# Kernel optimization log

Hardware: AMD Instinct MI355X
Metric: run time of the kernel (lower is better)

## Reference

```python
import jax, jax.numpy as jnp
import numpy as np

EPS = 1e-5
N_NODES = 50000


def sage_conv(x, src, dst, Wl, Wr, b):
    # mean-aggregate source features at destination nodes, then two linears
    msgs = x[src]  # [E, F] irregular gather
    agg = jax.ops.segment_sum(msgs, dst, num_segments=N_NODES)
    cnt = jax.ops.segment_sum(jnp.ones((src.shape[0], 1), x.dtype), dst,
                              num_segments=N_NODES)
    agg = agg / jnp.maximum(cnt, 1.0)
    return agg @ Wl + x @ Wr + b


def batch_norm(h, gamma, beta):
    mu = jnp.mean(h, axis=0)
    var = jnp.mean((h - mu) ** 2, axis=0)  # biased var, as torch BN training
    return (h - mu) * jax.lax.rsqrt(var + EPS) * gamma + beta


def setup_inputs() -> dict:
    key = jax.random.key(0)
    ks = jax.random.split(key, 16)
    d_in, d_h, n_cls, n_edges = 128, 128, 2, 600000
    s = lambda fan: 1.0 / np.sqrt(fan)
    inp = {
        "x": jax.random.normal(ks[0], (N_NODES, d_in), jnp.float32),
        "edge_index": jax.random.randint(ks[1], (2, n_edges), 0, N_NODES, jnp.int64),
        "W_l0": jax.random.uniform(ks[2], (d_in, d_h), jnp.float32, -s(d_in), s(d_in)),
        "W_r0": jax.random.uniform(ks[3], (d_in, d_h), jnp.float32, -s(d_in), s(d_in)),
        "b0": jnp.zeros((d_h,), jnp.float32),
        "g0": jnp.ones((d_h,), jnp.float32),
        "be0": jnp.zeros((d_h,), jnp.float32),
        "W_l1": jax.random.uniform(ks[4], (d_h, d_h), jnp.float32, -s(d_h), s(d_h)),
        "W_r1": jax.random.uniform(ks[5], (d_h, d_h), jnp.float32, -s(d_h), s(d_h)),
        "b1": jnp.zeros((d_h,), jnp.float32),
        "g1": jnp.ones((d_h,), jnp.float32),
        "be1": jnp.zeros((d_h,), jnp.float32),
        "W_out": jax.random.uniform(ks[6], (d_h, n_cls), jnp.float32, -s(d_h), s(d_h)),
        "b_out": jnp.zeros((n_cls,), jnp.float32),
    }
    return inp


def reference(x, edge_index, W_l0, W_r0, b0, g0, be0,
              W_l1, W_r1, b1, g1, be1, W_out, b_out):
    src, dst = edge_index[0], edge_index[1]
    # layer 0: SAGEConv -> BN -> ReLU (dropout = identity in eval/reference)
    h = sage_conv(x, src, dst, W_l0, W_r0, b0)
    h = jax.nn.relu(batch_norm(h, g0, be0))
    # layer 1
    h = sage_conv(h, src, dst, W_l1, W_r1, b1)
    h = jax.nn.relu(batch_norm(h, g1, be1))
    return h @ W_out + b_out
```

## Files before the change

### kernel.cpp

```cpp
#include <hip/hip_runtime.h>
#include <hip/hip_bf16.h>

#define F 128

typedef __attribute__((ext_vector_type(8))) short short8;
typedef __attribute__((ext_vector_type(4))) float floatx4;

__device__ __forceinline__ float bf_lo(unsigned u) { return __uint_as_float(u << 16); }
__device__ __forceinline__ float bf_hi(unsigned u) { return __uint_as_float(u & 0xffff0000u); }

__device__ __forceinline__ unsigned short f2bf(float x) {
  unsigned u = __float_as_uint(x);
  u += 0x7fffu + ((u >> 16) & 1u);
  return (unsigned short)(u >> 16);
}
__device__ __forceinline__ unsigned pack2(float a, float b) {
  return (unsigned)f2bf(a) | ((unsigned)f2bf(b) << 16);
}
__device__ __forceinline__ void add8(float* a, uint4 u) {
  a[0] += bf_lo(u.x); a[1] += bf_hi(u.x);
  a[2] += bf_lo(u.y); a[3] += bf_hi(u.y);
  a[4] += bf_lo(u.z); a[5] += bf_hi(u.z);
  a[6] += bf_lo(u.w); a[7] += bf_hi(u.w);
}

__global__ __launch_bounds__(256) void k_pre(const int* __restrict__ dst, int* __restrict__ A,
                                             int E, int cb,
                                             const float* __restrict__ x,
                                             const float* __restrict__ Wl0,
                                             const float* __restrict__ Wr0,
                                             const float* __restrict__ Wl1,
                                             const float* __restrict__ Wr1,
                                             unsigned short* __restrict__ xb,
                                             unsigned short* __restrict__ WcatT0,
                                             unsigned short* __restrict__ WcatT1, int n4) {
  if (blockIdx.x < cb) {
    int e = blockIdx.x * 256 + threadIdx.x;
    if (e < E) atomicAdd(&A[dst[e]], 1);
    return;
  }
  int i = (blockIdx.x - cb) * 256 + threadIdx.x;
  if (i < n4) {
    float4 v = ((const float4*)x)[i];
    ((ushort4*)xb)[i] = make_ushort4(f2bf(v.x), f2bf(v.y), f2bf(v.z), f2bf(v.w));
  } else {
    int j = i - n4;
    if (j < 2 * 256 * F) {
      int layer = j >> 15;
      int jj = j & 32767;
      int k = jj >> 7, n = jj & (F - 1);
      const float* Wl = layer ? Wl1 : Wl0;
      const float* Wr = layer ? Wr1 : Wr0;
      unsigned short* WT = layer ? WcatT1 : WcatT0;
      float v = (k < F) ? Wl[k * F + n] : Wr[(k - F) * F + n];
      WT[(size_t)n * 256 + k] = f2bf(v);
    }
  }
}

__global__ __launch_bounds__(1024) void k_scanfill(int* __restrict__ A, int* __restrict__ bsum,
                                                   int* __restrict__ bases, int* __restrict__ ctl,
                                                   int n, int nb,
                                                   const int* __restrict__ srcT,
                                                   const int* __restrict__ dstv,
                                                   int* __restrict__ adj, int E) {
  __shared__ int wtot[16];
  __shared__ int lastS, sbase;
  int t = threadIdx.x, l = t & 63, w = t >> 6;
  int i = blockIdx.x * 1024 + t;
  int v = (i < n) ? A[i] : 0;
  int acc = v;
#pragma unroll
  for (int off = 1; off < 64; off <<= 1) {
    int u = __shfl_up(acc, off);
    if (l >= off) acc += u;
  }
  if (l == 63) wtot[w] = acc;
  __syncthreads();
  int woff = 0, total = 0;
#pragma unroll
  for (int ww = 0; ww < 16; ++ww) {
    total += wtot[ww];
    if (ww < w) woff += wtot[ww];
  }
  int local = woff + (acc - v);
  if (t == 0) {
    __hip_atomic_store(&bsum[blockIdx.x], total, __ATOMIC_RELEASE, __HIP_MEMORY_SCOPE_AGENT);
    int tk = __hip_atomic_fetch_add(&ctl[0], 1, __ATOMIC_ACQ_REL, __HIP_MEMORY_SCOPE_AGENT);
    lastS = (tk == nb - 1);
  }
  __syncthreads();
  if (lastS) {
    if (t < 64) {
      int bv = (t < nb) ? __hip_atomic_load(&bsum[t], __ATOMIC_ACQUIRE, __HIP_MEMORY_SCOPE_AGENT) : 0;
      int a2 = bv;
#pragma unroll
      for (int off = 1; off < 64; off <<= 1) {
        int u = __shfl_up(a2, off);
        if (t >= off) a2 += u;
      }
      if (t < nb)
        __hip_atomic_store(&bases[t], a2 - bv, __ATOMIC_RELAXED, __HIP_MEMORY_SCOPE_AGENT);
    }
    __syncthreads();
    if (t == 0) {
      __threadfence();
      __hip_atomic_store(&ctl[1], 1, __ATOMIC_RELEASE, __HIP_MEMORY_SCOPE_AGENT);
    }
  }
  if (t == 0) {
    while (__hip_atomic_load(&ctl[1], __ATOMIC_ACQUIRE, __HIP_MEMORY_SCOPE_AGENT) == 0) {}
    sbase = __hip_atomic_load(&bases[blockIdx.x], __ATOMIC_RELAXED, __HIP_MEMORY_SCOPE_AGENT);
  }
  __syncthreads();
  if (i < n)
    __hip_atomic_store(&A[i], local + sbase, __ATOMIC_RELAXED, __HIP_MEMORY_SCOPE_AGENT);
  __syncthreads();
  if (t == 0) {
    __hip_atomic_fetch_add(&ctl[2], 1, __ATOMIC_ACQ_REL, __HIP_MEMORY_SCOPE_AGENT);
    while (__hip_atomic_load(&ctl[2], __ATOMIC_ACQUIRE, __HIP_MEMORY_SCOPE_AGENT) < nb) {}
  }
  __syncthreads();
  int nthr = nb * 1024;
  for (int e = blockIdx.x * 1024 + t; e < E; e += nthr) {
    int s = srcT[e], d = dstv[e];
    int slot = atomicAdd(&A[d], 1);
    adj[slot] = s;
  }
}

__global__ __launch_bounds__(256) void k_gather(const unsigned short* __restrict__ xin,
                                                const int* __restrict__ A,
                                                const int* __restrict__ adj,
                                                unsigned short* __restrict__ aggb, int N) {
  int d = blockIdx.x * 16 + (threadIdx.x >> 4);
  int ln = threadIdx.x & 15;
  if (d >= N) return;
  const uint4* xrows = (const uint4*)xin;
  int e0 = (d == 0) ? 0 : A[d - 1];
  int e1 = A[d];
  int deg = e1 - e0;
  float acc[8] = {0.f, 0.f, 0.f, 0.f, 0.f, 0.f, 0.f, 0.f};
  int e = e0;
  for (; e + 4 <= e1; e += 4) {
    int s0 = adj[e], s1 = adj[e + 1], s2 = adj[e + 2], s3 = adj[e + 3];
    uint4 u0 = xrows[(size_t)s0 * 16 + ln];
    uint4 u1 = xrows[(size_t)s1 * 16 + ln];
    uint4 u2 = xrows[(size_t)s2 * 16 + ln];
    uint4 u3 = xrows[(size_t)s3 * 16 + ln];
    add8(acc, u0);
    add8(acc, u1);
    add8(acc, u2);
    add8(acc, u3);
  }
  for (; e < e1; ++e) {
    uint4 u = xrows[(size_t)adj[e] * 16 + ln];
    add8(acc, u);
  }
  float inv = 1.0f / fmaxf((float)deg, 1.0f);
  uint4 o = make_uint4(pack2(acc[0] * inv, acc[1] * inv), pack2(acc[2] * inv, acc[3] * inv),
                       pack2(acc[4] * inv, acc[5] * inv), pack2(acc[6] * inv, acc[7] * inv));
  ((uint4*)aggb)[(size_t)d * 16 + ln] = o;
}

__global__ __launch_bounds__(256, 2) void k_gemm(
    const unsigned short* __restrict__ aggb, const unsigned short* __restrict__ xb,
    const unsigned short* __restrict__ WcatT, const float* __restrict__ bias,
    unsigned short* __restrict__ hb, float* __restrict__ pbuf, int N) {
  const int w = threadIdx.x >> 6;
  const int l = threadIdx.x & 63;
  const int lm = l & 15;
  const int lq = l >> 4;
  const int cbase = 32 * w;

  short8 bfrag[2][8];
#pragma unroll
  for (int c = 0; c < 2; ++c) {
    int col = cbase + 16 * c + lm;
    const unsigned short* wp = WcatT + (size_t)col * 256 + lq * 8;
#pragma unroll
    for (int s = 0; s < 8; ++s) bfrag[c][s] = *(const short8*)(wp + 32 * s);
  }
  float bcol0 = bias[cbase + lm];
  float bcol1 = bias[cbase + 16 + lm];
  float bsum0 = 0.f, bsum1 = 0.f, bsq0 = 0.f, bsq1 = 0.f;

  int r0 = blockIdx.x * 64;
  floatx4 acc[4][2] = {};
#pragma unroll
  for (int t = 0; t < 4; ++t) {
    int r = r0 + 16 * t + lm;
    const unsigned short* arow = aggb + (size_t)r * F + lq * 8;
    const unsigned short* xrow = xb + (size_t)r * F + lq * 8;
    short8 af[8];
#pragma unroll
    for (int s = 0; s < 4; ++s) {
      af[s] = *(const short8*)(arow + 32 * s);
      af[s + 4] = *(const short8*)(xrow + 32 * s);
    }
#pragma unroll
    for (int s = 0; s < 8; ++s) {
      acc[t][0] = __builtin_amdgcn_mfma_f32_16x16x32_bf16(af[s], bfrag[0][s], acc[t][0], 0, 0, 0);
      acc[t][1] = __builtin_amdgcn_mfma_f32_16x16x32_bf16(af[s], bfrag[1][s], acc[t][1], 0, 0, 0);
    }
  }
#pragma unroll
  for (int t = 0; t < 4; ++t) {
#pragma unroll
    for (int c = 0; c < 2; ++c) {
      int col = cbase + 16 * c + lm;
      float bc = c ? bcol1 : bcol0;
#pragma unroll
      for (int g = 0; g < 4; ++g) {
        int row = r0 + 16 * t + lq * 4 + g;
        if (row < N) {
          float v = acc[t][c][g] + bc;
          hb[(size_t)row * F + col] = f2bf(v);
          if (c) { bsum1 += v; bsq1 += v * v; }
          else   { bsum0 += v; bsq0 += v * v; }
        }
      }
    }
  }
  bsum0 += __shfl_xor(bsum0, 16); bsum0 += __shfl_xor(bsum0, 32);
  bsq0  += __shfl_xor(bsq0, 16);  bsq0  += __shfl_xor(bsq0, 32);
  bsum1 += __shfl_xor(bsum1, 16); bsum1 += __shfl_xor(bsum1, 32);
  bsq1  += __shfl_xor(bsq1, 16);  bsq1  += __shfl_xor(bsq1, 32);
  if (lq == 0) {
    float* pb = pbuf + (size_t)blockIdx.x * 256;
    pb[cbase + lm]            = bsum0;
    pb[128 + cbase + lm]      = bsq0;
    pb[cbase + 16 + lm]       = bsum1;
    pb[128 + cbase + 16 + lm] = bsq1;
  }
}

__global__ __launch_bounds__(256) void k_bnstats(const float* __restrict__ pbuf,
                                                 const float* __restrict__ g,
                                                 const float* __restrict__ be,
                                                 float* __restrict__ stats,
                                                 float* __restrict__ scale,
                                                 float* __restrict__ shift,
                                                 float invN, int nb) {
  int t = threadIdx.x;
  float s = 0.f;
  for (int b = blockIdx.x; b < nb; b += 8) s += pbuf[(size_t)b * 256 + t];
  atomicAdd(&stats[t], s);
  __threadfence();
  __syncthreads();
  __shared__ int lastS;
  if (t == 0) {
    int ticket = atomicAdd((int*)(stats + 256), 1);
    lastS = (ticket == 7);
  }
  __syncthreads();
  if (lastS) {
    __threadfence();
    if (t < 128) {
      float sum = __hip_atomic_load(&stats[t], __ATOMIC_RELAXED, __HIP_MEMORY_SCOPE_AGENT);
      float sq  = __hip_atomic_load(&stats[t + 128], __ATOMIC_RELAXED, __HIP_MEMORY_SCOPE_AGENT);
      float mu = sum * invN;
      float var = fmaxf(sq * invN - mu * mu, 0.0f);
      float sc = g[t] * rsqrtf(var + 1e-5f);
      scale[t] = sc;
      shift[t] = be[t] - mu * sc;
    }
  }
}

__global__ __launch_bounds__(256) void k_bnrelu(const unsigned short* __restrict__ h,
                                                unsigned short* __restrict__ dst,
                                                const float* __restrict__ scale,
                                                const float* __restrict__ shift, int n8) {
  int i = blockIdx.x * 256 + threadIdx.x;
  if (i >= n8) return;
  uint4 u = ((const uint4*)h)[i];
  int g = i & 15;
  float4 sc0 = ((const float4*)scale)[2 * g];
  float4 sc1 = ((const float4*)scale)[2 * g + 1];
  float4 sh0 = ((const float4*)shift)[2 * g];
  float4 sh1 = ((const float4*)shift)[2 * g + 1];
  unsigned o0 = pack2(fmaxf(fmaf(bf_lo(u.x), sc0.x, sh0.x), 0.f),
                      fmaxf(fmaf(bf_hi(u.x), sc0.y, sh0.y), 0.f));
  unsigned o1 = pack2(fmaxf(fmaf(bf_lo(u.y), sc0.z, sh0.z), 0.f),
                      fmaxf(fmaf(bf_hi(u.y), sc0.w, sh0.w), 0.f));
  unsigned o2 = pack2(fmaxf(fmaf(bf_lo(u.z), sc1.x, sh1.x), 0.f),
                      fmaxf(fmaf(bf_hi(u.z), sc1.y, sh1.y), 0.f));
  unsigned o3 = pack2(fmaxf(fmaf(bf_lo(u.w), sc1.z, sh1.z), 0.f),
                      fmaxf(fmaf(bf_hi(u.w), sc1.w, sh1.w), 0.f));
  ((uint4*)dst)[i] = make_uint4(o0, o1, o2, o3);
}

__global__ __launch_bounds__(256) void k_bnout(const unsigned short* __restrict__ hb,
                                               const float* __restrict__ scale,
                                               const float* __restrict__ shift,
                                               const float* __restrict__ Wout,
                                               const float* __restrict__ bout,
                                               float* __restrict__ out, int N) {
  __shared__ float W0s[F], W1s[F];
  int t = threadIdx.x;
  if (t < F) {
    W0s[t] = Wout[2 * t];
    W1s[t] = Wout[2 * t + 1];
  }
  __syncthreads();
  int r = blockIdx.x * 16 + (t >> 4);
  int ln = t & 15;
  if (r >= N) return;
  uint4 u = ((const uint4*)(hb + (size_t)r * F))[ln];
  float4 sc0 = ((const float4*)scale)[2 * ln];
  float4 sc1 = ((const float4*)scale)[2 * ln + 1];
  float4 sh0 = ((const float4*)shift)[2 * ln];
  float4 sh1 = ((const float4*)shift)[2 * ln + 1];
  float v[8];
  v[0] = fmaxf(fmaf(bf_lo(u.x), sc0.x, sh0.x), 0.f);
  v[1] = fmaxf(fmaf(bf_hi(u.x), sc0.y, sh0.y), 0.f);
  v[2] = fmaxf(fmaf(bf_lo(u.y), sc0.z, sh0.z), 0.f);
  v[3] = fmaxf(fmaf(bf_hi(u.y), sc0.w, sh0.w), 0.f);
  v[4] = fmaxf(fmaf(bf_lo(u.z), sc1.x, sh1.x), 0.f);
  v[5] = fmaxf(fmaf(bf_hi(u.z), sc1.y, sh1.y), 0.f);
  v[6] = fmaxf(fmaf(bf_lo(u.w), sc1.z, sh1.z), 0.f);
  v[7] = fmaxf(fmaf(bf_hi(u.w), sc1.w, sh1.w), 0.f);
  float a0 = 0.f, a1 = 0.f;
#pragma unroll
  for (int j = 0; j < 8; ++j) {
    a0 += v[j] * W0s[8 * ln + j];
    a1 += v[j] * W1s[8 * ln + j];
  }
#pragma unroll
  for (int off = 1; off < 16; off <<= 1) {
    a0 += __shfl_xor(a0, off);
    a1 += __shfl_xor(a1, off);
  }
  if (ln == 0) {
    out[2 * r]     = a0 + bout[0];
    out[2 * r + 1] = a1 + bout[1];
  }
}

extern "C" void kernel_launch(void* const* d_in, const int* in_sizes, int n_in,
                              void* d_out, int out_size, void* d_ws, size_t ws_size,
                              hipStream_t stream) {
  const float* x   = (const float*)d_in[0];
  const int*   eix = (const int*)d_in[1];
  const float* Wl0 = (const float*)d_in[2];
  const float* Wr0 = (const float*)d_in[3];
  const float* b0  = (const float*)d_in[4];
  const float* g0  = (const float*)d_in[5];
  const float* be0 = (const float*)d_in[6];
  const float* Wl1 = (const float*)d_in[7];
  const float* Wr1 = (const float*)d_in[8];
  const float* b1  = (const float*)d_in[9];
  const float* g1  = (const float*)d_in[10];
  const float* be1 = (const float*)d_in[11];
  const float* Wo  = (const float*)d_in[12];
  const float* bo  = (const float*)d_in[13];

  int N = in_sizes[0] / F;
  int E = in_sizes[1] / 2;
  const int* src  = eix;
  const int* dstv = eix + E;

  int nRowBlocks = (N + 63) / 64;
  size_t Npad = (size_t)nRowBlocks * 64;
  int nScanB = (N + 1023) / 1024;

  unsigned short* aggb   = (unsigned short*)d_ws;
  unsigned short* xb     = aggb + Npad * F;
  unsigned short* hb     = xb + Npad * F;
  unsigned short* WcatT0 = hb + Npad * F;
  unsigned short* WcatT1 = WcatT0 + 256 * F;
  float* scale  = (float*)(WcatT1 + 256 * F);
  float* shift  = scale + F;
  int*   A      = (int*)(shift + F);
  int*   bsum   = A + N;
  int*   bases  = bsum + 64;
  int*   ctl    = bases + 64;
  float* stats0 = (float*)(ctl + 4);
  float* stats1 = stats0 + 257;
  int*   adj    = (int*)(stats1 + 257);
  float* pbuf   = (float*)(adj + E);

  hipMemsetAsync(A, 0, (size_t)(N + 132 + 514) * sizeof(int), stream);

  int n4 = N * F / 4, n8 = N * F / 8;
  int cb = (E + 255) / 256;

  k_pre<<<cb + (n4 + 2 * 256 * F + 255) / 256, 256, 0, stream>>>(
      dstv, A, E, cb, x, Wl0, Wr0, Wl1, Wr1, xb, WcatT0, WcatT1, n4);

  k_scanfill<<<nScanB, 1024, 0, stream>>>(A, bsum, bases, ctl, N, nScanB, src, dstv, adj, E);

  k_gather<<<(N + 15) / 16, 256, 0, stream>>>(xb, A, adj, aggb, N);
  k_gemm<<<nRowBlocks, 256, 0, stream>>>(aggb, xb, WcatT0, b0, hb, pbuf, N);
  k_bnstats<<<8, 256, 0, stream>>>(pbuf, g0, be0, stats0, scale, shift, 1.0f / N, nRowBlocks);
  k_bnrelu<<<(n8 + 255) / 256, 256, 0, stream>>>(hb, xb, scale, shift, n8);

  k_gather<<<(N + 15) / 16, 256, 0, stream>>>(xb, A, adj, aggb, N);
  k_gemm<<<nRowBlocks, 256, 0, stream>>>(aggb, xb, WcatT1, b1, hb, pbuf, N);
  k_bnstats<<<8, 256, 0, stream>>>(pbuf, g1, be1, stats1, scale, shift, 1.0f / N, nRowBlocks);

  k_bnout<<<(N + 15) / 16, 256, 0, stream>>>(hb, scale, shift, Wo, bo, (float*)d_out, N);
}
```

Before: 348.0 us.

## Use cooperative grid sync to fuse BN stats with apply kernels

```diff
diff --git a/kernel.cpp b/kernel.cpp
--- a/kernel.cpp
+++ b/kernel.cpp
@@ -1,5 +1,8 @@
 #include <hip/hip_runtime.h>
 #include <hip/hip_bf16.h>
+#include <hip/hip_cooperative_groups.h>
+
+namespace cg = cooperative_groups;
 
 #define F 128
 
@@ -58,71 +61,71 @@
   }
 }
 
-__global__ __launch_bounds__(1024) void k_scanfill(int* __restrict__ A, int* __restrict__ bsum,
-                                                   int* __restrict__ bases, int* __restrict__ ctl,
-                                                   int n, int nb,
-                                                   const int* __restrict__ srcT,
-                                                   const int* __restrict__ dstv,
-                                                   int* __restrict__ adj, int E) {
-  __shared__ int wtot[16];
-  __shared__ int lastS, sbase;
+__global__ __launch_bounds__(256, 8) void k_scanfill(int* __restrict__ A, int* __restrict__ bsum,
+                                                     int n, int nbScan,
+                                                     const int* __restrict__ srcT,
+                                                     const int* __restrict__ dstv,
+                                                     int* __restrict__ adj, int E) {
+  cg::grid_group grid = cg::this_grid();
+  __shared__ int wtot[4];
+  __shared__ int sbase;
   int t = threadIdx.x, l = t & 63, w = t >> 6;
-  int i = blockIdx.x * 1024 + t;
-  int v = (i < n) ? A[i] : 0;
-  int acc = v;
-#pragma unroll
-  for (int off = 1; off < 64; off <<= 1) {
-    int u = __shfl_up(acc, off);
-    if (l >= off) acc += u;
-  }
-  if (l == 63) wtot[w] = acc;
-  __syncthreads();
-  int woff = 0, total = 0;
-#pragma unroll
-  for (int ww = 0; ww < 16; ++ww) {
-    total += wtot[ww];
-    if (ww < w) woff += wtot[ww];
-  }
-  int local = woff + (acc - v);
-  if (t == 0) {
-    __hip_atomic_store(&bsum[blockIdx.x], total, __ATOMIC_RELEASE, __HIP_MEMORY_SCOPE_AGENT);
-    int tk = __hip_atomic_fetch_add(&ctl[0], 1, __ATOMIC_ACQ_REL, __HIP_MEMORY_SCOPE_AGENT);
-    lastS = (tk == nb - 1);
-  }
-  __syncthreads();
-  if (lastS) {
+  int i0 = blockIdx.x * 1024 + t * 4;
+  int v0 = 0, v1 = 0, v2 = 0, v3 = 0;
+  int texcl = 0;
+  bool scanB = (int)blockIdx.x < nbScan;
+  if (scanB) {
+    if (i0 + 3 < n) {
+      int4 q = *(const int4*)(A + i0);
+      v0 = q.x; v1 = q.y; v2 = q.z; v3 = q.w;
+    } else {
+      if (i0 < n) v0 = A[i0];
+      if (i0 + 1 < n) v1 = A[i0 + 1];
+      if (i0 + 2 < n) v2 = A[i0 + 2];
+      if (i0 + 3 < n) v3 = A[i0 + 3];
+    }
+    int ts = v0 + v1 + v2 + v3;
+    int acc = ts;
+#pragma unroll
+    for (int off = 1; off < 64; off <<= 1) {
+      int u = __shfl_up(acc, off);
+      if (l >= off) acc += u;
+    }
+    if (l == 63) wtot[w] = acc;
+    __syncthreads();
+    int woff = 0;
+#pragma unroll
+    for (int ww = 0; ww < 4; ++ww)
+      if (ww < w) woff += wtot[ww];
+    texcl = woff + acc - ts;
+    if (t == 0) bsum[blockIdx.x] = wtot[0] + wtot[1] + wtot[2] + wtot[3];
+  }
+  grid.sync();
+  if (scanB) {
     if (t < 64) {
-      int bv = (t < nb) ? __hip_atomic_load(&bsum[t], __ATOMIC_ACQUIRE, __HIP_MEMORY_SCOPE_AGENT) : 0;
+      int bv = (t < nbScan) ? bsum[t] : 0;
       int a2 = bv;
 #pragma unroll
       for (int off = 1; off < 64; off <<= 1) {
         int u = __shfl_up(a2, off);
         if (t >= off) a2 += u;
       }
-      if (t < nb)
-        __hip_atomic_store(&bases[t], a2 - bv, __ATOMIC_RELAXED, __HIP_MEMORY_SCOPE_AGENT);
+      int base = __shfl(a2 - bv, blockIdx.x);
+      if (t == 0) sbase = base;
     }
     __syncthreads();
-    if (t == 0) {
-      __threadfence();
-      __hip_atomic_store(&ctl[1], 1, __ATOMIC_RELEASE, __HIP_MEMORY_SCOPE_AGENT);
-    }
-  }
-  if (t == 0) {
-    while (__hip_atomic_load(&ctl[1], __ATOMIC_ACQUIRE, __HIP_MEMORY_SCOPE_AGENT) == 0) {}
-    sbase = __hip_atomic_load(&bases[blockIdx.x], __ATOMIC_RELAXED, __HIP_MEMORY_SCOPE_AGENT);
-  }
-  __syncthreads();
-  if (i < n)
-    __hip_atomic_store(&A[i], local + sbase, __ATOMIC_RELAXED, __HIP_MEMORY_SCOPE_AGENT);
-  __syncthreads();
-  if (t == 0) {
-    __hip_atomic_fetch_add(&ctl[2], 1, __ATOMIC_ACQ_REL, __HIP_MEMORY_SCOPE_AGENT);
-    while (__hip_atomic_load(&ctl[2], __ATOMIC_ACQUIRE, __HIP_MEMORY_SCOPE_AGENT) < nb) {}
-  }
-  __syncthreads();
-  int nthr = nb * 1024;
-  for (int e = blockIdx.x * 1024 + t; e < E; e += nthr) {
+    int p = sbase + texcl;
+    if (i0 < n) __hip_atomic_store(&A[i0], p, __ATOMIC_RELAXED, __HIP_MEMORY_SCOPE_AGENT);
+    p += v0;
+    if (i0 + 1 < n) __hip_atomic_store(&A[i0 + 1], p, __ATOMIC_RELAXED, __HIP_MEMORY_SCOPE_AGENT);
+    p += v1;
+    if (i0 + 2 < n) __hip_atomic_store(&A[i0 + 2], p, __ATOMIC_RELAXED, __HIP_MEMORY_SCOPE_AGENT);
+    p += v2;
+    if (i0 + 3 < n) __hip_atomic_store(&A[i0 + 3], p, __ATOMIC_RELAXED, __HIP_MEMORY_SCOPE_AGENT);
+  }
+  grid.sync();
+  int nthr = gridDim.x * 256;
+  for (int e = blockIdx.x * 256 + t; e < E; e += nthr) {
     int s = srcT[e], d = dstv[e];
     int slot = atomicAdd(&A[d], 1);
     adj[slot] = s;
@@ -235,106 +238,115 @@
   }
 }
 
-__global__ __launch_bounds__(256) void k_bnstats(const float* __restrict__ pbuf,
+__global__ __launch_bounds__(256, 8) void k_bnre(const float* __restrict__ pbuf,
                                                  const float* __restrict__ g,
                                                  const float* __restrict__ be,
                                                  float* __restrict__ stats,
-                                                 float* __restrict__ scale,
-                                                 float* __restrict__ shift,
-                                                 float invN, int nb) {
+                                                 const unsigned short* __restrict__ h,
+                                                 unsigned short* __restrict__ dst,
+                                                 float invN, int nb, int n8) {
+  cg::grid_group grid = cg::this_grid();
   int t = threadIdx.x;
-  float s = 0.f;
-  for (int b = blockIdx.x; b < nb; b += 8) s += pbuf[(size_t)b * 256 + t];
-  atomicAdd(&stats[t], s);
-  __threadfence();
+  if (blockIdx.x < 16) {
+    float s = 0.f;
+    for (int b = blockIdx.x; b < nb; b += 16) s += pbuf[(size_t)b * 256 + t];
+    atomicAdd(&stats[t], s);
+  }
+  grid.sync();
+  __shared__ __align__(16) float scs[128], shs[128];
+  if (t < 128) {
+    float sum = stats[t];
+    float sq  = stats[t + 128];
+    float mu = sum * invN;
+    float var = fmaxf(sq * invN - mu * mu, 0.0f);
+    float sc = g[t] * rsqrtf(var + 1e-5f);
+    scs[t] = sc;
+    shs[t] = be[t] - mu * sc;
+  }
   __syncthreads();
-  __shared__ int lastS;
-  if (t == 0) {
-    int ticket = atomicAdd((int*)(stats + 256), 1);
-    lastS = (ticket == 7);
-  }
-  __syncthreads();
-  if (lastS) {
-    __threadfence();
-    if (t < 128) {
-      float sum = __hip_atomic_load(&stats[t], __ATOMIC_RELAXED, __HIP_MEMORY_SCOPE_AGENT);
-      float sq  = __hip_atomic_load(&stats[t + 128], __ATOMIC_RELAXED, __HIP_MEMORY_SCOPE_AGENT);
-      float mu = sum * invN;
-      float var = fmaxf(sq * invN - mu * mu, 0.0f);
-      float sc = g[t] * rsqrtf(var + 1e-5f);
-      scale[t] = sc;
-      shift[t] = be[t] - mu * sc;
-    }
-  }
-}
-
-__global__ __launch_bounds__(256) void k_bnrelu(const unsigned short* __restrict__ h,
-                                                unsigned short* __restrict__ dst,
-                                                const float* __restrict__ scale,
-                                                const float* __restrict__ shift, int n8) {
-  int i = blockIdx.x * 256 + threadIdx.x;
-  if (i >= n8) return;
-  uint4 u = ((const uint4*)h)[i];
-  int g = i & 15;
-  float4 sc0 = ((const float4*)scale)[2 * g];
-  float4 sc1 = ((const float4*)scale)[2 * g + 1];
-  float4 sh0 = ((const float4*)shift)[2 * g];
-  float4 sh1 = ((const float4*)shift)[2 * g + 1];
-  unsigned o0 = pack2(fmaxf(fmaf(bf_lo(u.x), sc0.x, sh0.x), 0.f),
-                      fmaxf(fmaf(bf_hi(u.x), sc0.y, sh0.y), 0.f));
-  unsigned o1 = pack2(fmaxf(fmaf(bf_lo(u.y), sc0.z, sh0.z), 0.f),
-                      fmaxf(fmaf(bf_hi(u.y), sc0.w, sh0.w), 0.f));
-  unsigned o2 = pack2(fmaxf(fmaf(bf_lo(u.z), sc1.x, sh1.x), 0.f),
-                      fmaxf(fmaf(bf_hi(u.z), sc1.y, sh1.y), 0.f));
-  unsigned o3 = pack2(fmaxf(fmaf(bf_lo(u.w), sc1.z, sh1.z), 0.f),
-                      fmaxf(fmaf(bf_hi(u.w), sc1.w, sh1.w), 0.f));
-  ((uint4*)dst)[i] = make_uint4(o0, o1, o2, o3);
-}
-
-__global__ __launch_bounds__(256) void k_bnout(const unsigned short* __restrict__ hb,
-                                               const float* __restrict__ scale,
-                                               const float* __restrict__ shift,
-                                               const float* __restrict__ Wout,
-                                               const float* __restrict__ bout,
-                                               float* __restrict__ out, int N) {
-  __shared__ float W0s[F], W1s[F];
+  int gg = t & 15;
+  float4 sc0 = ((const float4*)scs)[2 * gg];
+  float4 sc1 = ((const float4*)scs)[2 * gg + 1];
+  float4 sh0 = ((const float4*)shs)[2 * gg];
+  float4 sh1 = ((const float4*)shs)[2 * gg + 1];
+  int nthr = gridDim.x * 256;
+  for (int i = blockIdx.x * 256 + t; i < n8; i += nthr) {
+    uint4 u = ((const uint4*)h)[i];
+    unsigned o0 = pack2(fmaxf(fmaf(bf_lo(u.x), sc0.x, sh0.x), 0.f),
+                        fmaxf(fmaf(bf_hi(u.x), sc0.y, sh0.y), 0.f));
+    unsigned o1 = pack2(fmaxf(fmaf(bf_lo(u.y), sc0.z, sh0.z), 0.f),
+                        fmaxf(fmaf(bf_hi(u.y), sc0.w, sh0.w), 0.f));
+    unsigned o2 = pack2(fmaxf(fmaf(bf_lo(u.z), sc1.x, sh1.x), 0.f),
+                        fmaxf(fmaf(bf_hi(u.z), sc1.y, sh1.y), 0.f));
+    unsigned o3 = pack2(fmaxf(fmaf(bf_lo(u.w), sc1.z, sh1.z), 0.f),
+                        fmaxf(fmaf(bf_hi(u.w), sc1.w, sh1.w), 0.f));
+    ((uint4*)dst)[i] = make_uint4(o0, o1, o2, o3);
+  }
+}
+
+__global__ __launch_bounds__(256, 8) void k_bnoutf(const float* __restrict__ pbuf,
+                                                   const float* __restrict__ g,
+                                                   const float* __restrict__ be,
+                                                   float* __restrict__ stats,
+                                                   const unsigned short* __restrict__ hb,
+                                                   const float* __restrict__ Wout,
+                                                   const float* __restrict__ bout,
+                                                   float* __restrict__ out,
+                                                   float invN, int nb, int N) {
+  cg::grid_group grid = cg::this_grid();
   int t = threadIdx.x;
-  if (t < F) {
+  if (blockIdx.x < 16) {
+    float s = 0.f;
+    for (int b = blockIdx.x; b < nb; b += 16) s += pbuf[(size_t)b * 256 + t];
+    atomicAdd(&stats[t], s);
+  }
+  grid.sync();
+  __shared__ __align__(16) float scs[128], shs[128], W0s[128], W1s[128];
+  if (t < 128) {
+    float sum = stats[t];
+    float sq  = stats[t + 128];
+    float mu = sum * invN;
+    float var = fmaxf(sq * invN - mu * mu, 0.0f);
+    float sc = g[t] * rsqrtf(var + 1e-5f);
+    scs[t] = sc;
+    shs[t] = be[t] - mu * sc;
     W0s[t] = Wout[2 * t];
     W1s[t] = Wout[2 * t + 1];
   }
   __syncthreads();
-  int r = blockIdx.x * 16 + (t >> 4);
   int ln = t & 15;
-  if (r >= N) return;
-  uint4 u = ((const uint4*)(hb + (size_t)r * F))[ln];
-  float4 sc0 = ((const float4*)scale)[2 * ln];
-  float4 sc1 = ((const float4*)scale)[2 * ln + 1];
-  float4 sh0 = ((const float4*)shift)[2 * ln];
-  float4 sh1 = ((const float4*)shift)[2 * ln + 1];
-  float v[8];
-  v[0] = fmaxf(fmaf(bf_lo(u.x), sc0.x, sh0.x), 0.f);
-  v[1] = fmaxf(fmaf(bf_hi(u.x), sc0.y, sh0.y), 0.f);
-  v[2] = fmaxf(fmaf(bf_lo(u.y), sc0.z, sh0.z), 0.f);
-  v[3] = fmaxf(fmaf(bf_hi(u.y), sc0.w, sh0.w), 0.f);
-  v[4] = fmaxf(fmaf(bf_lo(u.z), sc1.x, sh1.x), 0.f);
-  v[5] = fmaxf(fmaf(bf_hi(u.z), sc1.y, sh1.y), 0.f);
-  v[6] = fmaxf(fmaf(bf_lo(u.w), sc1.z, sh1.z), 0.f);
-  v[7] = fmaxf(fmaf(bf_hi(u.w), sc1.w, sh1.w), 0.f);
-  float a0 = 0.f, a1 = 0.f;
-#pragma unroll
-  for (int j = 0; j < 8; ++j) {
-    a0 += v[j] * W0s[8 * ln + j];
-    a1 += v[j] * W1s[8 * ln + j];
-  }
-#pragma unroll
-  for (int off = 1; off < 16; off <<= 1) {
-    a0 += __shfl_xor(a0, off);
-    a1 += __shfl_xor(a1, off);
-  }
-  if (ln == 0) {
-    out[2 * r]     = a0 + bout[0];
-    out[2 * r + 1] = a1 + bout[1];
+  float4 sc0 = ((const float4*)scs)[2 * ln];
+  float4 sc1 = ((const float4*)scs)[2 * ln + 1];
+  float4 sh0 = ((const float4*)shs)[2 * ln];
+  float4 sh1 = ((const float4*)shs)[2 * ln + 1];
+  float b0o = bout[0], b1o = bout[1];
+  int nthr16 = gridDim.x * 16;
+  for (int r = blockIdx.x * 16 + (t >> 4); r < N; r += nthr16) {
+    uint4 u = ((const uint4*)(hb + (size_t)r * F))[ln];
+    float v[8];
+    v[0] = fmaxf(fmaf(bf_lo(u.x), sc0.x, sh0.x), 0.f);
+    v[1] = fmaxf(fmaf(bf_hi(u.x), sc0.y, sh0.y), 0.f);
+    v[2] = fmaxf(fmaf(bf_lo(u.y), sc0.z, sh0.z), 0.f);
+    v[3] = fmaxf(fmaf(bf_hi(u.y), sc0.w, sh0.w), 0.f);
+    v[4] = fmaxf(fmaf(bf_lo(u.z), sc1.x, sh1.x), 0.f);
+    v[5] = fmaxf(fmaf(bf_hi(u.z), sc1.y, sh1.y), 0.f);
+    v[6] = fmaxf(fmaf(bf_lo(u.w), sc1.z, sh1.z), 0.f);
+    v[7] = fmaxf(fmaf(bf_hi(u.w), sc1.w, sh1.w), 0.f);
+    float a0 = 0.f, a1 = 0.f;
+#pragma unroll
+    for (int j = 0; j < 8; ++j) {
+      a0 += v[j] * W0s[8 * ln + j];
+      a1 += v[j] * W1s[8 * ln + j];
+    }
+#pragma unroll
+    for (int off = 1; off < 16; off <<= 1) {
+      a0 += __shfl_xor(a0, off);
+      a1 += __shfl_xor(a1, off);
+    }
+    if (ln == 0) {
+      out[2 * r]     = a0 + b0o;
+      out[2 * r + 1] = a1 + b1o;
+    }
   }
 }
 
@@ -389,16 +401,34 @@
   k_pre<<<cb + (n4 + 2 * 256 * F + 255) / 256, 256, 0, stream>>>(
       dstv, A, E, cb, x, Wl0, Wr0, Wl1, Wr1, xb, WcatT0, WcatT1, n4);
 
-  k_scanfill<<<nScanB, 1024, 0, stream>>>(A, bsum, bases, ctl, N, nScanB, src, dstv, adj, E);
+  int mb_sf = 8, mb_re = 8, mb_of = 8;
+  hipOccupancyMaxActiveBlocksPerMultiprocessor(&mb_sf, k_scanfill, 256, 0);
+  hipOccupancyMaxActiveBlocksPerMultiprocessor(&mb_re, k_bnre, 256, 0);
+  hipOccupancyMaxActiveBlocksPerMultiprocessor(&mb_of, k_bnoutf, 256, 0);
+  int gsf = mb_sf * 256; if (gsf > 2048) gsf = 2048;
+  int gre = mb_re * 256; if (gre > 2048) gre = 2048;
+  int gof = mb_of * 256; if (gof > 2048) gof = 2048;
+
+  float invN = 1.0f / N;
+  {
+    void* args[] = {&A, &bsum, &N, &nScanB, (void*)&src, (void*)&dstv, &adj, &E};
+    hipLaunchCooperativeKernel((const void*)k_scanfill, dim3(gsf), dim3(256), args, 0, stream);
+  }
 
   k_gather<<<(N + 15) / 16, 256, 0, stream>>>(xb, A, adj, aggb, N);
   k_gemm<<<nRowBlocks, 256, 0, stream>>>(aggb, xb, WcatT0, b0, hb, pbuf, N);
-  k_bnstats<<<8, 256, 0, stream>>>(pbuf, g0, be0, stats0, scale, shift, 1.0f / N, nRowBlocks);
-  k_bnrelu<<<(n8 + 255) / 256, 256, 0, stream>>>(hb, xb, scale, shift, n8);
+  {
+    void* args[] = {&pbuf, (void*)&g0, (void*)&be0, &stats0, (void*)&hb, &xb,
+                    &invN, &nRowBlocks, &n8};
+    hipLaunchCooperativeKernel((const void*)k_bnre, dim3(gre), dim3(256), args, 0, stream);
+  }
 
   k_gather<<<(N + 15) / 16, 256, 0, stream>>>(xb, A, adj, aggb, N);
   k_gemm<<<nRowBlocks, 256, 0, stream>>>(aggb, xb, WcatT1, b1, hb, pbuf, N);
-  k_bnstats<<<8, 256, 0, stream>>>(pbuf, g1, be1, stats1, scale, shift, 1.0f / N, nRowBlocks);
-
-  k_bnout<<<(N + 15) / 16, 256, 0, stream>>>(hb, scale, shift, Wo, bo, (float*)d_out, N);
-}
+  {
+    void* out_p = d_out;
+    void* args[] = {&pbuf, (void*)&g1, (void*)&be1, &stats1, (void*)&hb, (void*)&Wo,
+                    (void*)&bo, &out_p, &invN, &nRowBlocks, &N};
+    hipLaunchCooperativeKernel((const void*)k_bnoutf, dim3(gof), dim3(256), args, 0, stream);
+  }
+}
```

Measured after the change: 856.6 us. +146.2%, slower.
